# Optimization experiments

Measured on AMD Instinct MI355X. Metric: run time of the kernel, lower is better.

Reference implementation:

```python
import jax, jax.numpy as jnp
import numpy as np

B, N, F, C, HD = 16, 2048, 1024, 256, 64  # batch, points, feat_dims, channels, head dim
EPS_BN = 1e-5

def conv1d(w, x, b=None):
    # 1x1 Conv1d: w [O,C], x [B,C,N] -> [B,O,N]
    y = jnp.einsum('oc,bcn->bon', w, x)
    return y if b is None else y + b[None, :, None]

def batchnorm(x, g, b):
    # training-mode BN over (batch, length) per channel, biased variance
    m = x.mean(axis=(0, 2), keepdims=True)
    v = x.var(axis=(0, 2), keepdims=True)
    return g[None, :, None] * (x - m) * jax.lax.rsqrt(v + EPS_BN) + b[None, :, None]

def leaky(x):
    return jnp.where(x > 0, x, 0.2 * x)

def oa_layer(x, qk_w, qk_b, v_w, v_b, t_w, t_b, bn_g, bn_b):
    # x: [B,256,N]; q and k share weights (q_conv.weight = k_conv.weight)
    q = conv1d(qk_w, x, qk_b).transpose(0, 2, 1)      # [B,N,64]
    k = conv1d(qk_w, x, qk_b)                         # [B,64,N]
    v = conv1d(v_w, x, v_b)                           # [B,256,N]
    energy = jnp.einsum('bnc,bcm->bnm', q, k)         # [B,N,N]
    att = jax.nn.softmax(energy, axis=-1)
    att = att / (1e-9 + att.sum(axis=1, keepdims=True))  # L1 renorm over columns
    x_r = jnp.einsum('bcn,bnm->bcm', v, att)          # [B,256,N]
    x_r = leaky(batchnorm(conv1d(t_w, x - x_r, t_b), bn_g, bn_b))
    return x + x_r

def setup_inputs() -> dict:
    key = jax.random.key(0)
    ks = jax.random.split(key, 20)
    s = lambda fan: 1.0 / np.sqrt(fan)
    inp = {
        'feature': jax.random.normal(ks[0], (B, 1, F), jnp.float32),
        'prior': jax.random.normal(ks[1], (B, 3, N), jnp.float32),
        'mlp_w': jax.random.normal(ks[2], (C, F + 3), jnp.float32) * s(F + 3),
        'mlp_b': jax.random.normal(ks[3], (C,), jnp.float32) * 0.01,
        'qk_w': jax.random.normal(ks[4], (4, HD, C), jnp.float32) * s(C),
        'qk_b': jax.random.normal(ks[5], (4, HD), jnp.float32) * 0.01,
        'v_w': jax.random.normal(ks[6], (4, C, C), jnp.float32) * s(C),
        'v_b': jax.random.normal(ks[7], (4, C), jnp.float32) * 0.01,
        't_w': jax.random.normal(ks[8], (4, C, C), jnp.float32) * s(C),
        't_b': jax.random.normal(ks[9], (4, C), jnp.float32) * 0.01,
        'bn_g': jnp.ones((4, C), jnp.float32),
        'bn_b': jnp.zeros((4, C), jnp.float32),
        'dc1_w': jax.random.normal(ks[10], (C, 4 * C), jnp.float32) * s(4 * C),
        'dc1_bn_g': jnp.ones((C,), jnp.float32),
        'dc1_bn_b': jnp.zeros((C,), jnp.float32),
        'dc2_w': jax.random.normal(ks[11], (3, C), jnp.float32) * s(C),
        'dc2_b': jax.random.normal(ks[12], (3,), jnp.float32) * 0.01,
        'dc2_bn_g': jnp.ones((3,), jnp.float32),
        'dc2_bn_b': jnp.zeros((3,), jnp.float32),
    }
    return inp

def reference(feature, prior, mlp_w, mlp_b, qk_w, qk_b, v_w, v_b, t_w, t_b,
              bn_g, bn_b, dc1_w, dc1_bn_g, dc1_bn_b, dc2_w, dc2_b,
              dc2_bn_g, dc2_bn_b):
    n = prior.shape[2]
    feat = jnp.broadcast_to(feature.transpose(0, 2, 1), (feature.shape[0], feature.shape[2], n))
    p = conv1d(mlp_w, jnp.concatenate([feat, prior], axis=1), mlp_b)  # [B,256,N]
    outs = []
    for i in range(4):
        p = oa_layer(p, qk_w[i], qk_b[i], v_w[i], v_b[i], t_w[i], t_b[i], bn_g[i], bn_b[i])
        outs.append(p)
    pc = jnp.concatenate(outs, axis=1)                                # [B,1024,N]
    h = leaky(batchnorm(conv1d(dc1_w, pc), dc1_bn_g, dc1_bn_b))
    points = jnp.tanh(batchnorm(conv1d(dc2_w, h, dc2_b), dc2_bn_g, dc2_bn_b))
    return points.transpose(0, 2, 1)                                  # [B,N,3]
```

## Files before the change

### kernel.cpp

```cpp
#include <hip/hip_runtime.h>
#include <hip/hip_bf16.h>

typedef __hip_bfloat16 bf16;
typedef unsigned short ushort_t;

constexpr int kB = 16;
constexpr int kN = 2048;
constexpr int kF = 1024;
constexpr int kC = 256;
constexpr int kH = 64;

using f32x4 = __attribute__((ext_vector_type(4))) float;
using bf16x8 = __attribute__((ext_vector_type(8))) short;

__device__ __forceinline__ float us2f(unsigned short u) {
  union { unsigned int i; float f; } w;
  w.i = ((unsigned int)u) << 16;
  return w.f;
}
__device__ __forceinline__ unsigned short f2bu(float f) {
  union { bf16 h; unsigned short s; } u;
  u.h = __float2bfloat16(f);
  return u.s;
}

__global__ __launch_bounds__(256) void k_fb(const float* __restrict__ feat,
                                            const float* __restrict__ mlp_w,
                                            const float* __restrict__ mlp_b,
                                            float* __restrict__ fb) {
  const int b = blockIdx.x >> 8;
  const int c = blockIdx.x & 255;
  const int t = threadIdx.x;
  const float* wr = mlp_w + (size_t)c * (kF + 3);
  const float* fr = feat + (size_t)b * kF;
  float s = 0.f;
  for (int f = t; f < kF; f += 256) s += wr[f] * fr[f];
  __shared__ float red[256];
  red[t] = s;
  __syncthreads();
  for (int k = 128; k > 0; k >>= 1) {
    if (t < k) red[t] += red[t + k];
    __syncthreads();
  }
  if (t == 0) fb[blockIdx.x] = red[0] + mlp_b[c];
}

__global__ __launch_bounds__(256) void k_p0(const float* __restrict__ prior,
                                            const float* __restrict__ mlp_w,
                                            const float* __restrict__ fb,
                                            ushort_t* __restrict__ psh,
                                            ushort_t* __restrict__ psl) {
  const size_t i = (size_t)blockIdx.x * 256 + threadIdx.x;
  const int c = (int)(i & 255);
  const int n = (int)((i >> 8) & 2047);
  const int b = (int)(i >> 19);
  const float* wr = mlp_w + (size_t)c * (kF + 3) + kF;
  const float* pr = prior + (size_t)b * 3 * kN + n;
  const float v = fb[b * kC + c] + wr[0] * pr[0] + wr[1] * pr[kN] + wr[2] * pr[2 * kN];
  const ushort_t h = f2bu(v);
  psh[i] = h;
  psl[i] = f2bu(v - us2f(h));
}

__global__ __launch_bounds__(256) void k_wsplit(const float* __restrict__ qk_w,
                                                const float* __restrict__ v_w,
                                                const float* __restrict__ t_w,
                                                const float* __restrict__ dc1_w,
                                                ushort_t* __restrict__ wfh,
                                                ushort_t* __restrict__ wfl) {
  const int idx = blockIdx.x * 256 + threadIdx.x;
  const float* src;
  int stride, OS_;
  size_t dstoff;
  int g;
  if (idx < 8192) {
    const int l = idx >> 11; g = idx & 2047;
    src = qk_w + (size_t)l * 64 * 256; stride = 256; OS_ = 4;
    dstoff = (size_t)l * 16384;
  } else if (idx < 40960) {
    const int i2 = idx - 8192; const int l = i2 >> 13; g = i2 & 8191;
    src = v_w + (size_t)l * 256 * 256; stride = 256; OS_ = 16;
    dstoff = 65536 + (size_t)l * 65536;
  } else if (idx < 73728) {
    const int i2 = idx - 40960; const int l = i2 >> 13; g = i2 & 8191;
    src = t_w + (size_t)l * 256 * 256; stride = 256; OS_ = 16;
    dstoff = 327680 + (size_t)l * 65536;
  } else {
    const int i2 = idx - 73728; const int l = i2 >> 13; g = i2 & 8191;
    src = dc1_w + (size_t)l * 256; stride = 1024; OS_ = 16;
    dstoff = 589824 + (size_t)l * 65536;
  }
  const int kk = g / (OS_ * 64);
  const int rem = g % (OS_ * 64);
  const int osub = rem >> 6;
  const int lane = rem & 63;
  const int o = osub * 16 + (lane & 15);
  const int c = kk * 32 + (lane >> 4) * 8;
  const float* sp = src + (size_t)o * stride + c;
  ushort_t h[8], l8[8];
#pragma unroll
  for (int j = 0; j < 8; ++j) {
    const float v = sp[j];
    h[j] = f2bu(v);
    l8[j] = f2bu(v - us2f(h[j]));
  }
  *(uint4*)(wfh + dstoff + (size_t)g * 8) = *(const uint4*)h;
  *(uint4*)(wfl + dstoff + (size_t)g * 8) = *(const uint4*)l8;
}

__global__ __launch_bounds__(256) void k_qv(
    const ushort_t* __restrict__ xh, const ushort_t* __restrict__ xl,
    const ushort_t* __restrict__ wqh, const ushort_t* __restrict__ wql,
    const ushort_t* __restrict__ wvh, const ushort_t* __restrict__ wvl,
    const float* __restrict__ qbias, const float* __restrict__ vbias,
    ushort_t* __restrict__ Qh, ushort_t* __restrict__ Ql,
    bf16* __restrict__ Vo) {
  const int t = threadIdx.x;
  const int b = blockIdx.y;
  const int n0 = blockIdx.x * 64;
  const int lane = t & 63, wv = t >> 6;
  const int fr = lane & 15, fq = lane >> 4;
  const ushort_t* xbh = xh + ((size_t)b * kN + n0) * kC;
  const ushort_t* xbl = xl + ((size_t)b * kN + n0) * kC;
  f32x4 accq[4];
  f32x4 accv[4][4];
#pragma unroll
  for (int ns = 0; ns < 4; ++ns) {
    accq[ns] = (f32x4){0.f, 0.f, 0.f, 0.f};
#pragma unroll
    for (int s = 0; s < 4; ++s) accv[s][ns] = (f32x4){0.f, 0.f, 0.f, 0.f};
  }
  for (int kk = 0; kk < 8; ++kk) {
    bf16x8 bh[4], bl[4];
#pragma unroll
    for (int ns = 0; ns < 4; ++ns) {
      const size_t xi = (size_t)(ns * 16 + fr) * kC + kk * 32 + fq * 8;
      bh[ns] = *(const bf16x8*)(xbh + xi);
      bl[ns] = *(const bf16x8*)(xbl + xi);
    }
    {
      const size_t wi = (((size_t)kk * 4 + wv) * 64 + lane) * 8;
      const bf16x8 ah = *(const bf16x8*)(wqh + wi);
      const bf16x8 al = *(const bf16x8*)(wql + wi);
#pragma unroll
      for (int ns = 0; ns < 4; ++ns) {
        accq[ns] = __builtin_amdgcn_mfma_f32_16x16x32_bf16(ah, bh[ns], accq[ns], 0, 0, 0);
        accq[ns] = __builtin_amdgcn_mfma_f32_16x16x32_bf16(ah, bl[ns], accq[ns], 0, 0, 0);
        accq[ns] = __builtin_amdgcn_mfma_f32_16x16x32_bf16(al, bh[ns], accq[ns], 0, 0, 0);
      }
    }
#pragma unroll
    for (int s = 0; s < 4; ++s) {
      const size_t wi = (((size_t)kk * 16 + wv * 4 + s) * 64 + lane) * 8;
      const bf16x8 ah = *(const bf16x8*)(wvh + wi);
      const bf16x8 al = *(const bf16x8*)(wvl + wi);
#pragma unroll
      for (int ns = 0; ns < 4; ++ns) {
        accv[s][ns] = __builtin_amdgcn_mfma_f32_16x16x32_bf16(ah, bh[ns], accv[s][ns], 0, 0, 0);
        accv[s][ns] = __builtin_amdgcn_mfma_f32_16x16x32_bf16(ah, bl[ns], accv[s][ns], 0, 0, 0);
        accv[s][ns] = __builtin_amdgcn_mfma_f32_16x16x32_bf16(al, bh[ns], accv[s][ns], 0, 0, 0);
      }
    }
  }
  {
    const int o0 = wv * 16 + fq * 4;
#pragma unroll
    for (int ns = 0; ns < 4; ++ns) {
      const int n = n0 + ns * 16 + fr;
      ushort_t h4[4], l4[4];
#pragma unroll
      for (int r = 0; r < 4; ++r) {
        const float v = accq[ns][r] + qbias[o0 + r];
        h4[r] = f2bu(v);
        l4[r] = f2bu(v - us2f(h4[r]));
      }
      *(ushort4*)(Qh + ((size_t)b * kN + n) * kH + o0) = *(const ushort4*)h4;
      *(ushort4*)(Ql + ((size_t)b * kN + n) * kH + o0) = *(const ushort4*)l4;
    }
  }
#pragma unroll
  for (int s = 0; s < 4; ++s) {
    const int o0 = (wv * 4 + s) * 16 + fq * 4;
#pragma unroll
    for (int ns = 0; ns < 4; ++ns) {
      const int n = n0 + ns * 16 + fr;
#pragma unroll
      for (int r = 0; r < 4; ++r)
        Vo[((size_t)b * kC + o0 + r) * kN + n] = __float2bfloat16(accv[s][ns][r] + vbias[o0 + r]);
    }
  }
}

template <int O, int MODE>
__global__ __launch_bounds__(256) void k_conv(
    const ushort_t* __restrict__ xh, const ushort_t* __restrict__ xl,
    const ushort_t* __restrict__ wfh, const ushort_t* __restrict__ wfl,
    const float* __restrict__ bias,
    ushort_t* __restrict__ o1, ushort_t* __restrict__ o2,
    float* __restrict__ of) {
  constexpr int KK = 8;
  constexpr int OS = O / 16;
  constexpr int OSW = OS / 4;
  const int t = threadIdx.x;
  const int b = blockIdx.y;
  const int n0 = blockIdx.x * 64;
  const int lane = t & 63, wv = t >> 6;
  const int fr = lane & 15, fq = lane >> 4;
  const ushort_t* xbh = xh + ((size_t)b * kN + n0) * kC;
  const ushort_t* xbl = xl + ((size_t)b * kN + n0) * kC;
  f32x4 acc[OSW][4];
#pragma unroll
  for (int s = 0; s < OSW; ++s)
#pragma unroll
    for (int ns = 0; ns < 4; ++ns) acc[s][ns] = (f32x4){0.f, 0.f, 0.f, 0.f};
  for (int kk = 0; kk < KK; ++kk) {
    bf16x8 bh[4], bl[4];
#pragma unroll
    for (int ns = 0; ns < 4; ++ns) {
      const size_t xi = (size_t)(ns * 16 + fr) * kC + kk * 32 + fq * 8;
      bh[ns] = *(const bf16x8*)(xbh + xi);
      bl[ns] = *(const bf16x8*)(xbl + xi);
    }
#pragma unroll
    for (int s = 0; s < OSW; ++s) {
      const size_t wi = (((size_t)kk * OS + wv * OSW + s) * 64 + lane) * 8;
      const bf16x8 ah = *(const bf16x8*)(wfh + wi);
      const bf16x8 al = *(const bf16x8*)(wfl + wi);
#pragma unroll
      for (int ns = 0; ns < 4; ++ns) {
        acc[s][ns] = __builtin_amdgcn_mfma_f32_16x16x32_bf16(ah, bh[ns], acc[s][ns], 0, 0, 0);
        acc[s][ns] = __builtin_amdgcn_mfma_f32_16x16x32_bf16(ah, bl[ns], acc[s][ns], 0, 0, 0);
        acc[s][ns] = __builtin_amdgcn_mfma_f32_16x16x32_bf16(al, bh[ns], acc[s][ns], 0, 0, 0);
      }
    }
  }
  if (MODE == 2) {
    const int blk = blockIdx.y * gridDim.x + blockIdx.x;
#pragma unroll
    for (int s = 0; s < OSW; ++s) {
      const int o0 = (wv * OSW + s) * 16 + fq * 4;
      float yv[4][4];
#pragma unroll
      for (int ns = 0; ns < 4; ++ns) {
        const int n = n0 + ns * 16 + fr;
        const size_t idx = ((size_t)b * kN + n) * kC + o0;
        ushort_t h4[4], l4[4];
#pragma unroll
        for (int r = 0; r < 4; ++r) {
          const float y = acc[s][ns][r] + bias[o0 + r];
          yv[ns][r] = y;
          h4[r] = f2bu(y);
          l4[r] = f2bu(y - us2f(h4[r]));
        }
        *(ushort4*)(o1 + idx) = *(const ushort4*)h4;
        *(ushort4*)(o2 + idx) = *(const ushort4*)l4;
      }
#pragma unroll
      for (int r = 0; r < 4; ++r) {
        float s1 = yv[0][r] + yv[1][r] + yv[2][r] + yv[3][r];
        float s2 = yv[0][r] * yv[0][r] + yv[1][r] * yv[1][r] +
                   yv[2][r] * yv[2][r] + yv[3][r] * yv[3][r];
#pragma unroll
        for (int mask = 1; mask < 16; mask <<= 1) {
          s1 += __shfl_xor(s1, mask);
          s2 += __shfl_xor(s2, mask);
        }
        if (fr == 0) {
          of[(size_t)(o0 + r) * 512 + blk] = s1;
          of[131072 + (size_t)(o0 + r) * 512 + blk] = s2;
        }
      }
    }
  } else {
#pragma unroll
    for (int s = 0; s < OSW; ++s) {
      const int o0 = (wv * OSW + s) * 16 + fq * 4;
#pragma unroll
      for (int ns = 0; ns < 4; ++ns) {
        const int n = n0 + ns * 16 + fr;
#pragma unroll
        for (int r = 0; r < 4; ++r) {
          float* pp = of + ((size_t)b * kC + o0 + r) * kN + n;
          *pp = *pp + acc[s][ns][r];
        }
      }
    }
  }
}

__global__ __launch_bounds__(128) void k_bnred(const float* __restrict__ part,
                                               const float* __restrict__ g,
                                               const float* __restrict__ bb,
                                               float* __restrict__ af,
                                               float* __restrict__ cf) {
  const int c = blockIdx.x, t = threadIdx.x;
  const float4 v1 = *(const float4*)&part[(size_t)c * 512 + t * 4];
  const float4 v2 = *(const float4*)&part[131072 + (size_t)c * 512 + t * 4];
  float s1 = v1.x + v1.y + v1.z + v1.w;
  float s2 = v2.x + v2.y + v2.z + v2.w;
  __shared__ float r1[128], r2[128];
  r1[t] = s1;
  r2[t] = s2;
  __syncthreads();
  for (int k = 64; k > 0; k >>= 1) {
    if (t < k) {
      r1[t] += r1[t + k];
      r2[t] += r2[t + k];
    }
    __syncthreads();
  }
  if (t == 0) {
    const float im = 1.f / (float)(kB * kN);
    const float m = r1[0] * im;
    const float var = r2[0] * im - m * m;
    const float a = g[c] * rsqrtf(var + 1e-5f);
    af[c] = a;
    cf[c] = bb[c] - a * m;
  }
}

__global__ __launch_bounds__(256) void k_bnapply2(const ushort_t* __restrict__ yh,
                                                  const ushort_t* __restrict__ yl,
                                                  ushort_t* __restrict__ ph,
                                                  ushort_t* __restrict__ pl,
                                                  const float* __restrict__ af,
                                                  const float* __restrict__ cf) {
  const size_t i = ((size_t)blockIdx.x * 256 + threadIdx.x) * 4;
  const int c0 = (int)(i & 255);
  const ushort4 yh4 = *(const ushort4*)(yh + i);
  const ushort4 yl4 = *(const ushort4*)(yl + i);
  const ushort4 ph4 = *(const ushort4*)(ph + i);
  const ushort4 pl4 = *(const ushort4*)(pl + i);
  const float4 a4 = *(const float4*)(af + c0);
  const float4 c4 = *(const float4*)(cf + c0);
  const float y0 = us2f(yh4.x) + us2f(yl4.x);
  const float y1 = us2f(yh4.y) + us2f(yl4.y);
  const float y2 = us2f(yh4.z) + us2f(yl4.z);
  const float y3 = us2f(yh4.w) + us2f(yl4.w);
  float z0 = a4.x * y0 + c4.x; z0 = z0 > 0.f ? z0 : 0.2f * z0;
  float z1 = a4.y * y1 + c4.y; z1 = z1 > 0.f ? z1 : 0.2f * z1;
  float z2 = a4.z * y2 + c4.z; z2 = z2 > 0.f ? z2 : 0.2f * z2;
  float z3 = a4.w * y3 + c4.w; z3 = z3 > 0.f ? z3 : 0.2f * z3;
  const float p0 = us2f(ph4.x) + us2f(pl4.x) + z0;
  const float p1 = us2f(ph4.y) + us2f(pl4.y) + z1;
  const float p2 = us2f(ph4.z) + us2f(pl4.z) + z2;
  const float p3 = us2f(ph4.w) + us2f(pl4.w) + z3;
  ushort4 nh, nl;
  nh.x = f2bu(p0); nl.x = f2bu(p0 - us2f(nh.x));
  nh.y = f2bu(p1); nl.y = f2bu(p1 - us2f(nh.y));
  nh.z = f2bu(p2); nl.z = f2bu(p2 - us2f(nh.z));
  nh.w = f2bu(p3); nl.w = f2bu(p3 - us2f(nh.w));
  *(ushort4*)(ph + i) = nh;
  *(ushort4*)(pl + i) = nl;
}

__global__ __launch_bounds__(256) void k_rowstats(const ushort_t* __restrict__ Qhi,
                                                  const ushort_t* __restrict__ Qlo,
                                                  float* __restrict__ rmx,
                                                  float* __restrict__ rsn) {
  __shared__ __align__(16) ushort_t Bh[2][64][72];
  __shared__ __align__(16) ushort_t Bl[2][64][72];
  const int b = blockIdx.y, t = threadIdx.x;
  const int r0 = blockIdx.x * 64;
  const int lane = t & 63, w = t >> 6;
  const int fr = lane & 15, fq = lane >> 4;
  const size_t qbase = (size_t)b * kN * kH;
  bf16x8 ah0, ah1, al0, al1;
  {
    const ushort_t* qh = Qhi + qbase + (size_t)(r0 + w * 16 + fr) * kH;
    const ushort_t* ql = Qlo + qbase + (size_t)(r0 + w * 16 + fr) * kH;
    ah0 = *(const bf16x8*)(qh + fq * 8);
    ah1 = *(const bf16x8*)(qh + 32 + fq * 8);
    al0 = *(const bf16x8*)(ql + fq * 8);
    al1 = *(const bf16x8*)(ql + 32 + fq * 8);
  }
  float mx[4] = {-3.0e38f, -3.0e38f, -3.0e38f, -3.0e38f};
  float sm[4] = {0.f, 0.f, 0.f, 0.f};
  const int srow = t >> 2, scol = (t & 3) * 16;
  {
    const ushort_t* qh = Qhi + qbase + (size_t)srow * kH + scol;
    const ushort_t* ql = Qlo + qbase + (size_t)srow * kH + scol;
    *(uint4*)&Bh[0][srow][scol] = *(const uint4*)qh;
    *(uint4*)&Bh[0][srow][scol + 8] = *(const uint4*)(qh + 8);
    *(uint4*)&Bl[0][srow][scol] = *(const uint4*)ql;
    *(uint4*)&Bl[0][srow][scol + 8] = *(const uint4*)(ql + 8);
  }
  __syncthreads();
  int cur = 0;
  for (int m0 = 0; m0 < kN; m0 += 64) {
    uint4 rh0, rh1, rl0, rl1;
    const bool pf = (m0 + 64 < kN);
    if (pf) {
      const ushort_t* qh = Qhi + qbase + (size_t)(m0 + 64 + srow) * kH + scol;
      const ushort_t* ql = Qlo + qbase + (size_t)(m0 + 64 + srow) * kH + scol;
      rh0 = *(const uint4*)qh;
      rh1 = *(const uint4*)(qh + 8);
      rl0 = *(const uint4*)ql;
      rl1 = *(const uint4*)(ql + 8);
    }
    float ev[4][4];
#pragma unroll
    for (int cs = 0; cs < 4; ++cs) {
      const bf16x8 bh0 = *(const bf16x8*)&Bh[cur][cs * 16 + fr][fq * 8];
      const bf16x8 bh1 = *(const bf16x8*)&Bh[cur][cs * 16 + fr][32 + fq * 8];
      const bf16x8 bl0 = *(const bf16x8*)&Bl[cur][cs * 16 + fr][fq * 8];
      const bf16x8 bl1 = *(const bf16x8*)&Bl[cur][cs * 16 + fr][32 + fq * 8];
      f32x4 e = {0.f, 0.f, 0.f, 0.f};
      e = __builtin_amdgcn_mfma_f32_16x16x32_bf16(ah0, bh0, e, 0, 0, 0);
      e = __builtin_amdgcn_mfma_f32_16x16x32_bf16(ah1, bh1, e, 0, 0, 0);
      e = __builtin_amdgcn_mfma_f32_16x16x32_bf16(ah0, bl0, e, 0, 0, 0);
      e = __builtin_amdgcn_mfma_f32_16x16x32_bf16(ah1, bl1, e, 0, 0, 0);
      e = __builtin_amdgcn_mfma_f32_16x16x32_bf16(al0, bh0, e, 0, 0, 0);
      e = __builtin_amdgcn_mfma_f32_16x16x32_bf16(al1, bh1, e, 0, 0, 0);
      ev[cs][0] = e[0]; ev[cs][1] = e[1]; ev[cs][2] = e[2]; ev[cs][3] = e[3];
    }
#pragma unroll
    for (int r = 0; r < 4; ++r) {
      const float tmax = fmaxf(fmaxf(ev[0][r], ev[1][r]), fmaxf(ev[2][r], ev[3][r]));
      const float nm = fmaxf(mx[r], tmax);
      sm[r] = sm[r] * __expf(mx[r] - nm) + __expf(ev[0][r] - nm) + __expf(ev[1][r] - nm) +
              __expf(ev[2][r] - nm) + __expf(ev[3][r] - nm);
      mx[r] = nm;
    }
    if (pf) {
      *(uint4*)&Bh[cur ^ 1][srow][scol] = rh0;
      *(uint4*)&Bh[cur ^ 1][srow][scol + 8] = rh1;
      *(uint4*)&Bl[cur ^ 1][srow][scol] = rl0;
      *(uint4*)&Bl[cur ^ 1][srow][scol + 8] = rl1;
    }
    __syncthreads();
    cur ^= 1;
  }
#pragma unroll
  for (int mask = 1; mask < 16; mask <<= 1) {
#pragma unroll
    for (int r = 0; r < 4; ++r) {
      const float om = __shfl_xor(mx[r], mask);
      const float os = __shfl_xor(sm[r], mask);
      const float nm = fmaxf(mx[r], om);
      sm[r] = sm[r] * __expf(mx[r] - nm) + os * __expf(om - nm);
      mx[r] = nm;
    }
  }
  if (fr == 0) {
#pragma unroll
    for (int r = 0; r < 4; ++r) {
      const int row = r0 + w * 16 + fq * 4 + r;
      rmx[(size_t)b * kN + row] = mx[r];
      rsn[(size_t)b * kN + row] = 1.f / sm[r];
    }
  }
}

__global__ __launch_bounds__(256) void k_colpass(const ushort_t* __restrict__ Qhi,
                                                 const ushort_t* __restrict__ Qlo,
                                                 const bf16* __restrict__ V,
                                                 const float* __restrict__ rmx,
                                                 const float* __restrict__ rsn,
                                                 const ushort_t* __restrict__ psh,
                                                 const ushort_t* __restrict__ psl,
                                                 ushort_t* __restrict__ ush,
                                                 ushort_t* __restrict__ usl) {
  constexpr int MT = 64, NT = 32;
  __shared__ __align__(16) ushort_t Anh[2][NT][72];
  __shared__ __align__(16) ushort_t Anl[2][NT][72];
  __shared__ __align__(16) ushort_t Vs[2][kC][40];
  __shared__ __align__(16) ushort_t Pl[MT][40];
  __shared__ float CsI[MT];
  const int t = threadIdx.x;
  const int b = blockIdx.y;
  const int mBase = blockIdx.x * MT;
  const size_t qbase = (size_t)b * kN * kH;
  const ushort_t* Vb_ = (const ushort_t*)V + (size_t)b * kC * kN;
  const int lane = t & 63, wv = t >> 6;
  const int fr = lane & 15, fq = lane >> 4;
  bf16x8 bmh0, bmh1, bml0, bml1;
  {
    const ushort_t* qh = Qhi + qbase + (size_t)(mBase + wv * 16 + fr) * kH;
    const ushort_t* ql = Qlo + qbase + (size_t)(mBase + wv * 16 + fr) * kH;
    bmh0 = *(const bf16x8*)(qh + fq * 8);
    bmh1 = *(const bf16x8*)(qh + 32 + fq * 8);
    bml0 = *(const bf16x8*)(ql + fq * 8);
    bml1 = *(const bf16x8*)(ql + 32 + fq * 8);
  }
  f32x4 acc[4][4];
#pragma unroll
  for (int i = 0; i < 4; ++i)
#pragma unroll
    for (int j = 0; j < 4; ++j) acc[i][j] = (f32x4){0.f, 0.f, 0.f, 0.f};
  float csloc = 0.f;
  const int arow = t >> 3, acol = (t & 7) * 8;
  const int vc = t >> 2, vq = t & 3;
  {
    *(uint4*)&Anh[0][arow][acol] = *(const uint4*)(Qhi + qbase + (size_t)arow * kH + acol);
    *(uint4*)&Anl[0][arow][acol] = *(const uint4*)(Qlo + qbase + (size_t)arow * kH + acol);
#pragma unroll
    for (int it = 0; it < 4; ++it) {
      const int c = it * 64 + vc;
      *(uint4*)&Vs[0][c][vq * 8] = *(const uint4*)(Vb_ + (size_t)c * kN + vq * 8);
    }
  }
  __syncthreads();
  int cur = 0;
  for (int n0 = 0; n0 < kN; n0 += NT) {
    uint4 rAh, rAl, rV0, rV1, rV2, rV3;
    const bool pf = (n0 + NT < kN);
    if (pf) {
      const int nn = n0 + NT;
      rAh = *(const uint4*)(Qhi + qbase + (size_t)(nn + arow) * kH + acol);
      rAl = *(const uint4*)(Qlo + qbase + (size_t)(nn + arow) * kH + acol);
      rV0 = *(const uint4*)(Vb_ + (size_t)(0 * 64 + vc) * kN + nn + vq * 8);
      rV1 = *(const uint4*)(Vb_ + (size_t)(1 * 64 + vc) * kN + nn + vq * 8);
      rV2 = *(const uint4*)(Vb_ + (size_t)(2 * 64 + vc) * kN + nn + vq * 8);
      rV3 = *(const uint4*)(Vb_ + (size_t)(3 * 64 + vc) * kN + nn + vq * 8);
    }
    const float4 rm0 = *(const float4*)&rmx[(size_t)b * kN + n0 + fq * 4];
    const float4 rm1 = *(const float4*)&rmx[(size_t)b * kN + n0 + 16 + fq * 4];
    const float4 rs0 = *(const float4*)&rsn[(size_t)b * kN + n0 + fq * 4];
    const float4 rs1 = *(const float4*)&rsn[(size_t)b * kN + n0 + 16 + fq * 4];
#pragma unroll
    for (int ns = 0; ns < 2; ++ns) {
      const bf16x8 ah0 = *(const bf16x8*)&Anh[cur][ns * 16 + fr][fq * 8];
      const bf16x8 ah1 = *(const bf16x8*)&Anh[cur][ns * 16 + fr][32 + fq * 8];
      const bf16x8 al0 = *(const bf16x8*)&Anl[cur][ns * 16 + fr][fq * 8];
      const bf16x8 al1 = *(const bf16x8*)&Anl[cur][ns * 16 + fr][32 + fq * 8];
      f32x4 e = {0.f, 0.f, 0.f, 0.f};
      e = __builtin_amdgcn_mfma_f32_16x16x32_bf16(ah0, bmh0, e, 0, 0, 0);
      e = __builtin_amdgcn_mfma_f32_16x16x32_bf16(ah1, bmh1, e, 0, 0, 0);
      e = __builtin_amdgcn_mfma_f32_16x16x32_bf16(ah0, bml0, e, 0, 0, 0);
      e = __builtin_amdgcn_mfma_f32_16x16x32_bf16(ah1, bml1, e, 0, 0, 0);
      e = __builtin_amdgcn_mfma_f32_16x16x32_bf16(al0, bmh0, e, 0, 0, 0);
      e = __builtin_amdgcn_mfma_f32_16x16x32_bf16(al1, bmh1, e, 0, 0, 0);
      const float4 rm = ns ? rm1 : rm0;
      const float4 rs = ns ? rs1 : rs0;
      ushort_t p4[4];
      {
        const float p0 = __expf(e[0] - rm.x) * rs.x;
        const float p1 = __expf(e[1] - rm.y) * rs.y;
        const float p2 = __expf(e[2] - rm.z) * rs.z;
        const float p3 = __expf(e[3] - rm.w) * rs.w;
        p4[0] = f2bu(p0); p4[1] = f2bu(p1); p4[2] = f2bu(p2); p4[3] = f2bu(p3);
        csloc += p0 + p1 + p2 + p3;
      }
      *(ushort4*)&Pl[wv * 16 + fr][ns * 16 + fq * 4] = *(const ushort4*)p4;
    }
    __syncthreads();
    bf16x8 am[4], bv[4];
#pragma unroll
    for (int ms = 0; ms < 4; ++ms)
      am[ms] = *(const bf16x8*)&Pl[ms * 16 + fr][fq * 8];
#pragma unroll
    for (int cs = 0; cs < 4; ++cs)
      bv[cs] = *(const bf16x8*)&Vs[cur][wv * 64 + cs * 16 + fr][fq * 8];
#pragma unroll
    for (int ms = 0; ms < 4; ++ms)
#pragma unroll
      for (int cs = 0; cs < 4; ++cs)
        acc[ms][cs] = __builtin_amdgcn_mfma_f32_16x16x32_bf16(am[ms], bv[cs], acc[ms][cs], 0, 0, 0);
    if (pf) {
      *(uint4*)&Anh[cur ^ 1][arow][acol] = rAh;
      *(uint4*)&Anl[cur ^ 1][arow][acol] = rAl;
      *(uint4*)&Vs[cur ^ 1][0 * 64 + vc][vq * 8] = rV0;
      *(uint4*)&Vs[cur ^ 1][1 * 64 + vc][vq * 8] = rV1;
      *(uint4*)&Vs[cur ^ 1][2 * 64 + vc][vq * 8] = rV2;
      *(uint4*)&Vs[cur ^ 1][3 * 64 + vc][vq * 8] = rV3;
    }
    __syncthreads();
    cur ^= 1;
  }
  csloc += __shfl_xor(csloc, 16);
  csloc += __shfl_xor(csloc, 32);
  if (fq == 0) CsI[wv * 16 + fr] = 1.f / (1e-9f + csloc);
  __syncthreads();
#pragma unroll
  for (int ms = 0; ms < 4; ++ms) {
#pragma unroll
    for (int r = 0; r < 4; ++r) {
      const int ml = ms * 16 + fq * 4 + r;
      const float inv = CsI[ml];
      const size_t row = ((size_t)b * kN + mBase + ml) * kC;
#pragma unroll
      for (int cs = 0; cs < 4; ++cs) {
        const int c = wv * 64 + cs * 16 + fr;
        const float xv = us2f(psh[row + c]) + us2f(psl[row + c]);
        const float u = xv - acc[ms][cs][r] * inv;
        const ushort_t h = f2bu(u);
        ush[row + c] = h;
        usl[row + c] = f2bu(u - us2f(h));
      }
    }
  }
}

__global__ __launch_bounds__(256) void k_bnstats(const float* __restrict__ y, int nch,
                                                 float* __restrict__ mean,
                                                 float* __restrict__ rsig) {
  const int c = blockIdx.x, t = threadIdx.x;
  float s = 0.f, s2 = 0.f;
  for (int b = 0; b < kB; ++b) {
    const float* p = y + ((size_t)b * nch + c) * kN;
    for (int n = t; n < kN; n += 256) {
      const float v = p[n];
      s += v;
      s2 += v * v;
    }
  }
  __shared__ float r1[256], r2[256];
  r1[t] = s;
  r2[t] = s2;
  __syncthreads();
  for (int k = 128; k > 0; k >>= 1) {
    if (t < k) {
      r1[t] += r1[t + k];
      r2[t] += r2[t + k];
    }
    __syncthreads();
  }
  if (t == 0) {
    const float im = 1.f / (float)(kB * kN);
    const float m = r1[0] * im;
    const float var = r2[0] * im - m * m;
    mean[c] = m;
    rsig[c] = rsqrtf(var + 1e-5f);
  }
}

__global__ __launch_bounds__(256) void k_dc2(const float* __restrict__ h,
                                             const float* __restrict__ mean,
                                             const float* __restrict__ rsig,
                                             const float* __restrict__ g,
                                             const float* __restrict__ bb,
                                             const float* __restrict__ w,
                                             const float* __restrict__ d2b,
                                             float* __restrict__ tpre) {
  __shared__ float wS[3][kC];
  __shared__ float aS[kC], cS[kC];
  const int t = threadIdx.x, b = blockIdx.y;
  const int n = blockIdx.x * 256 + t;
  {
    const float a = g[t] * rsig[t];
    aS[t] = a;
    cS[t] = bb[t] - a * mean[t];
    wS[0][t] = w[t];
    wS[1][t] = w[kC + t];
    wS[2][t] = w[2 * kC + t];
  }
  __syncthreads();
  float a0 = d2b[0], a1 = d2b[1], a2 = d2b[2];
  const float* hb = h + (size_t)b * kC * kN + n;
  for (int c = 0; c < kC; ++c) {
    float z = hb[(size_t)c * kN] * aS[c] + cS[c];
    z = z > 0.f ? z : 0.2f * z;
    a0 += wS[0][c] * z;
    a1 += wS[1][c] * z;
    a2 += wS[2][c] * z;
  }
  tpre[((size_t)b * 3 + 0) * kN + n] = a0;
  tpre[((size_t)b * 3 + 1) * kN + n] = a1;
  tpre[((size_t)b * 3 + 2) * kN + n] = a2;
}

__global__ __launch_bounds__(256) void k_final(const float* __restrict__ tpre,
                                               const float* __restrict__ mean,
                                               const float* __restrict__ rsig,
                                               const float* __restrict__ g,
                                               const float* __restrict__ bb,
                                               float* __restrict__ out) {
  const int i = blockIdx.x * 256 + threadIdx.x;
  const int n = i & (kN - 1), b = i >> 11;
#pragma unroll
  for (int j = 0; j < 3; ++j) {
    const float v = tpre[((size_t)b * 3 + j) * kN + n];
    const float z = g[j] * (v - mean[j]) * rsig[j] + bb[j];
    out[(size_t)i * 3 + j] = tanhf(z);
  }
}

extern "C" void kernel_launch(void* const* d_in, const int* in_sizes, int n_in,
                              void* d_out, int out_size, void* d_ws, size_t ws_size,
                              hipStream_t stream) {
  const float* feature  = (const float*)d_in[0];
  const float* prior    = (const float*)d_in[1];
  const float* mlp_w    = (const float*)d_in[2];
  const float* mlp_b    = (const float*)d_in[3];
  const float* qk_w     = (const float*)d_in[4];
  const float* qk_b     = (const float*)d_in[5];
  const float* v_w      = (const float*)d_in[6];
  const float* v_b      = (const float*)d_in[7];
  const float* t_w      = (const float*)d_in[8];
  const float* t_b      = (const float*)d_in[9];
  const float* bn_g     = (const float*)d_in[10];
  const float* bn_b     = (const float*)d_in[11];
  const float* dc1_w    = (const float*)d_in[12];
  const float* dc1_bn_g = (const float*)d_in[13];
  const float* dc1_bn_b = (const float*)d_in[14];
  const float* dc2_w    = (const float*)d_in[15];
  const float* dc2_b    = (const float*)d_in[16];
  const float* dc2_bn_g = (const float*)d_in[17];
  const float* dc2_bn_b = (const float*)d_in[18];
  float* out = (float*)d_out;

  char* base = (char*)d_ws;
  size_t off = 0;
  auto carve = [&](size_t bytes) {
    char* p = base + off;
    off += (bytes + 255) & ~(size_t)255;
    return p;
  };
  const size_t ne = (size_t)kB * kN * kC;
  ushort_t* psh  = (ushort_t*)carve(ne * 2);
  ushort_t* psl  = (ushort_t*)carve(ne * 2);
  ushort_t* ush  = (ushort_t*)carve(ne * 2);
  ushort_t* usl  = (ushort_t*)carve(ne * 2);
  float*    hacc = (float*)carve(ne * 4);
  ushort_t* Qhi  = (ushort_t*)carve((size_t)kB * kN * kH * 2);
  ushort_t* Qlo  = (ushort_t*)carve((size_t)kB * kN * kH * 2);
  bf16*     Vb   = (bf16*)carve(ne * 2);
  ushort_t* wfh  = (ushort_t*)carve((size_t)851968 * 2);
  ushort_t* wfl  = (ushort_t*)carve((size_t)851968 * 2);
  float*    part = (float*)carve((size_t)2 * 131072 * 4);
  float*    rmx  = (float*)carve((size_t)kB * kN * 4);
  float*    rsn  = (float*)carve((size_t)kB * kN * 4);
  float*    fb   = (float*)carve((size_t)kB * kC * 4);
  float*    bnm  = (float*)carve(kC * 4);
  float*    bnr  = (float*)carve(kC * 4);
  float*    tpre = (float*)carve((size_t)kB * 3 * kN * 4);

  hipMemsetAsync(hacc, 0, ne * 4, stream);
  k_wsplit<<<416, 256, 0, stream>>>(qk_w, v_w, t_w, dc1_w, wfh, wfl);
  k_fb<<<kB * kC, 256, 0, stream>>>(feature, mlp_w, mlp_b, fb);
  k_p0<<<(int)(ne / 256), 256, 0, stream>>>(prior, mlp_w, fb, psh, psl);

  const dim3 gC(kN / 64, kB);
  for (int l = 0; l < 4; ++l) {
    const size_t qk_off  = (size_t)l * 16384;
    const size_t v_off   = 65536 + (size_t)l * 65536;
    const size_t t_off   = 327680 + (size_t)l * 65536;
    const size_t dc1_off = 589824 + (size_t)l * 65536;
    k_qv<<<gC, 256, 0, stream>>>(psh, psl, wfh + qk_off, wfl + qk_off,
                                 wfh + v_off, wfl + v_off,
                                 qk_b + l * kH, v_b + l * kC, Qhi, Qlo, Vb);
    k_rowstats<<<gC, 256, 0, stream>>>(Qhi, Qlo, rmx, rsn);
    k_colpass<<<gC, 256, 0, stream>>>(Qhi, Qlo, Vb, rmx, rsn, psh, psl, ush, usl);
    k_conv<256, 2><<<gC, 256, 0, stream>>>(ush, usl, wfh + t_off, wfl + t_off,
                                           t_b + l * kC, ush, usl, part);
    k_bnred<<<kC, 128, 0, stream>>>(part, bn_g + l * kC, bn_b + l * kC, bnm, bnr);
    k_bnapply2<<<(int)(ne / 4 / 256), 256, 0, stream>>>(ush, usl, psh, psl, bnm, bnr);
    k_conv<256, 4><<<gC, 256, 0, stream>>>(psh, psl, wfh + dc1_off, wfl + dc1_off,
                                           nullptr, nullptr, nullptr, hacc);
  }

  k_bnstats<<<kC, 256, 0, stream>>>(hacc, kC, bnm, bnr);
  k_dc2<<<dim3(kN / 256, kB), 256, 0, stream>>>(hacc, bnm, bnr, dc1_bn_g, dc1_bn_b,
                                                dc2_w, dc2_b, tpre);
  k_bnstats<<<3, 256, 0, stream>>>(tpre, 3, bnm, bnr);
  k_final<<<(kB * kN) / 256, 256, 0, stream>>>(tpre, bnm, bnr, dc2_bn_g, dc2_bn_b, out);
}
```

Before: 1.234 ms.

## Fuse BN-apply residual, dc1 conv, and next-layer QV projection into one kernel

Replaces the separate BN-apply, dc1 conv and next-layer Q/V projection kernels with one fused kernel. Each block computes the updated residual in registers, feeds it straight into the MFMA GEMMs for dc1 and for the next layer's Q/V, and has one wave write the updated p back. This removes a full read/write pass over the activations and two launches per layer. In exchange the fused kernel holds many accumulators (Q, V and dc1), so register pressure rises and occupancy may drop.

```diff
diff --git a/kernel.cpp b/kernel.cpp
--- a/kernel.cpp
+++ b/kernel.cpp
@@ -191,16 +191,158 @@
   }
 }
 
-template <int O, int MODE>
-__global__ __launch_bounds__(256) void k_conv(
+template <int HASQV>
+__global__ __launch_bounds__(256, 2) void k_fuse(
+    const ushort_t* __restrict__ yh, const ushort_t* __restrict__ yl,
+    ushort_t* __restrict__ ph, ushort_t* __restrict__ pl,
+    const float* __restrict__ af, const float* __restrict__ cf,
+    const ushort_t* __restrict__ wqh, const ushort_t* __restrict__ wql,
+    const ushort_t* __restrict__ wvh, const ushort_t* __restrict__ wvl,
+    const ushort_t* __restrict__ wdh, const ushort_t* __restrict__ wdl,
+    const float* __restrict__ qbias, const float* __restrict__ vbias,
+    ushort_t* __restrict__ Qh, ushort_t* __restrict__ Ql,
+    bf16* __restrict__ Vo, float* __restrict__ hacc) {
+  const int t = threadIdx.x;
+  const int b = blockIdx.y;
+  const int n0 = blockIdx.x * 64;
+  const int lane = t & 63, wv = t >> 6;
+  const int fr = lane & 15, fq = lane >> 4;
+  const size_t rowbase = ((size_t)b * kN + n0) * kC;
+  f32x4 accq[4];
+  f32x4 accv[4][4];
+  f32x4 accd[4][4];
+#pragma unroll
+  for (int ns = 0; ns < 4; ++ns) {
+    accq[ns] = (f32x4){0.f, 0.f, 0.f, 0.f};
+#pragma unroll
+    for (int s = 0; s < 4; ++s) {
+      accv[s][ns] = (f32x4){0.f, 0.f, 0.f, 0.f};
+      accd[s][ns] = (f32x4){0.f, 0.f, 0.f, 0.f};
+    }
+  }
+  for (int kk = 0; kk < 8; ++kk) {
+    const int cbase = kk * 32 + fq * 8;
+    const float4 a4a = *(const float4*)(af + cbase);
+    const float4 a4b = *(const float4*)(af + cbase + 4);
+    const float4 c4a = *(const float4*)(cf + cbase);
+    const float4 c4b = *(const float4*)(cf + cbase + 4);
+    const float av[8] = {a4a.x, a4a.y, a4a.z, a4a.w, a4b.x, a4b.y, a4b.z, a4b.w};
+    const float cv[8] = {c4a.x, c4a.y, c4a.z, c4a.w, c4b.x, c4b.y, c4b.z, c4b.w};
+    bf16x8 bh[4], bl[4];
+#pragma unroll
+    for (int ns = 0; ns < 4; ++ns) {
+      const size_t idx = rowbase + (size_t)(ns * 16 + fr) * kC + cbase;
+      ushort_t yh8[8], yl8[8], p8h[8], p8l[8], nh8[8], nl8[8];
+      *(uint4*)yh8 = *(const uint4*)(yh + idx);
+      *(uint4*)yl8 = *(const uint4*)(yl + idx);
+      *(uint4*)p8h = *(const uint4*)(ph + idx);
+      *(uint4*)p8l = *(const uint4*)(pl + idx);
+#pragma unroll
+      for (int j = 0; j < 8; ++j) {
+        const float yv = us2f(yh8[j]) + us2f(yl8[j]);
+        float z = av[j] * yv + cv[j];
+        z = z > 0.f ? z : 0.2f * z;
+        const float pv = us2f(p8h[j]) + us2f(p8l[j]) + z;
+        nh8[j] = f2bu(pv);
+        nl8[j] = f2bu(pv - us2f(nh8[j]));
+      }
+      bh[ns] = *(const bf16x8*)nh8;
+      bl[ns] = *(const bf16x8*)nl8;
+    }
+    __syncthreads();
+    if (wv == 0) {
+#pragma unroll
+      for (int ns = 0; ns < 4; ++ns) {
+        const size_t idx = rowbase + (size_t)(ns * 16 + fr) * kC + cbase;
+        *(uint4*)(ph + idx) = *(const uint4*)&bh[ns];
+        *(uint4*)(pl + idx) = *(const uint4*)&bl[ns];
+      }
+    }
+    if (HASQV) {
+      const size_t wi = (((size_t)kk * 4 + wv) * 64 + lane) * 8;
+      const bf16x8 ah = *(const bf16x8*)(wqh + wi);
+      const bf16x8 al = *(const bf16x8*)(wql + wi);
+#pragma unroll
+      for (int ns = 0; ns < 4; ++ns) {
+        accq[ns] = __builtin_amdgcn_mfma_f32_16x16x32_bf16(ah, bh[ns], accq[ns], 0, 0, 0);
+        accq[ns] = __builtin_amdgcn_mfma_f32_16x16x32_bf16(ah, bl[ns], accq[ns], 0, 0, 0);
+        accq[ns] = __builtin_amdgcn_mfma_f32_16x16x32_bf16(al, bh[ns], accq[ns], 0, 0, 0);
+      }
+#pragma unroll
+      for (int s = 0; s < 4; ++s) {
+        const size_t wi2 = (((size_t)kk * 16 + wv * 4 + s) * 64 + lane) * 8;
+        const bf16x8 vh = *(const bf16x8*)(wvh + wi2);
+        const bf16x8 vl = *(const bf16x8*)(wvl + wi2);
+#pragma unroll
+        for (int ns = 0; ns < 4; ++ns) {
+          accv[s][ns] = __builtin_amdgcn_mfma_f32_16x16x32_bf16(vh, bh[ns], accv[s][ns], 0, 0, 0);
+          accv[s][ns] = __builtin_amdgcn_mfma_f32_16x16x32_bf16(vh, bl[ns], accv[s][ns], 0, 0, 0);
+          accv[s][ns] = __builtin_amdgcn_mfma_f32_16x16x32_bf16(vl, bh[ns], accv[s][ns], 0, 0, 0);
+        }
+      }
+    }
+#pragma unroll
+    for (int s = 0; s < 4; ++s) {
+      const size_t wi3 = (((size_t)kk * 16 + wv * 4 + s) * 64 + lane) * 8;
+      const bf16x8 dh = *(const bf16x8*)(wdh + wi3);
+      const bf16x8 dl = *(const bf16x8*)(wdl + wi3);
+#pragma unroll
+      for (int ns = 0; ns < 4; ++ns) {
+        accd[s][ns] = __builtin_amdgcn_mfma_f32_16x16x32_bf16(dh, bh[ns], accd[s][ns], 0, 0, 0);
+        accd[s][ns] = __builtin_amdgcn_mfma_f32_16x16x32_bf16(dh, bl[ns], accd[s][ns], 0, 0, 0);
+        accd[s][ns] = __builtin_amdgcn_mfma_f32_16x16x32_bf16(dl, bh[ns], accd[s][ns], 0, 0, 0);
+      }
+    }
+  }
+  if (HASQV) {
+    const int o0 = wv * 16 + fq * 4;
+#pragma unroll
+    for (int ns = 0; ns < 4; ++ns) {
+      const int n = n0 + ns * 16 + fr;
+      ushort_t h4[4], l4[4];
+#pragma unroll
+      for (int r = 0; r < 4; ++r) {
+        const float v = accq[ns][r] + qbias[o0 + r];
+        h4[r] = f2bu(v);
+        l4[r] = f2bu(v - us2f(h4[r]));
+      }
+      *(ushort4*)(Qh + ((size_t)b * kN + n) * kH + o0) = *(const ushort4*)h4;
+      *(ushort4*)(Ql + ((size_t)b * kN + n) * kH + o0) = *(const ushort4*)l4;
+    }
+#pragma unroll
+    for (int s = 0; s < 4; ++s) {
+      const int oV = (wv * 4 + s) * 16 + fq * 4;
+#pragma unroll
+      for (int ns = 0; ns < 4; ++ns) {
+        const int n = n0 + ns * 16 + fr;
+#pragma unroll
+        for (int r = 0; r < 4; ++r)
+          Vo[((size_t)b * kC + oV + r) * kN + n] =
+              __float2bfloat16(accv[s][ns][r] + vbias[oV + r]);
+      }
+    }
+  }
+#pragma unroll
+  for (int s = 0; s < 4; ++s) {
+    const int oD = (wv * 4 + s) * 16 + fq * 4;
+#pragma unroll
+    for (int ns = 0; ns < 4; ++ns) {
+      const int n = n0 + ns * 16 + fr;
+#pragma unroll
+      for (int r = 0; r < 4; ++r) {
+        float* pp = hacc + ((size_t)b * kC + oD + r) * kN + n;
+        *pp = *pp + accd[s][ns][r];
+      }
+    }
+  }
+}
+
+__global__ __launch_bounds__(256) void k_tconv(
     const ushort_t* __restrict__ xh, const ushort_t* __restrict__ xl,
     const ushort_t* __restrict__ wfh, const ushort_t* __restrict__ wfl,
     const float* __restrict__ bias,
     ushort_t* __restrict__ o1, ushort_t* __restrict__ o2,
     float* __restrict__ of) {
-  constexpr int KK = 8;
-  constexpr int OS = O / 16;
-  constexpr int OSW = OS / 4;
   const int t = threadIdx.x;
   const int b = blockIdx.y;
   const int n0 = blockIdx.x * 64;
@@ -208,12 +350,12 @@
   const int fr = lane & 15, fq = lane >> 4;
   const ushort_t* xbh = xh + ((size_t)b * kN + n0) * kC;
   const ushort_t* xbl = xl + ((size_t)b * kN + n0) * kC;
-  f32x4 acc[OSW][4];
-#pragma unroll
-  for (int s = 0; s < OSW; ++s)
+  f32x4 acc[4][4];
+#pragma unroll
+  for (int s = 0; s < 4; ++s)
 #pragma unroll
     for (int ns = 0; ns < 4; ++ns) acc[s][ns] = (f32x4){0.f, 0.f, 0.f, 0.f};
-  for (int kk = 0; kk < KK; ++kk) {
+  for (int kk = 0; kk < 8; ++kk) {
     bf16x8 bh[4], bl[4];
 #pragma unroll
     for (int ns = 0; ns < 4; ++ns) {
@@ -222,8 +364,8 @@
       bl[ns] = *(const bf16x8*)(xbl + xi);
     }
 #pragma unroll
-    for (int s = 0; s < OSW; ++s) {
-      const size_t wi = (((size_t)kk * OS + wv * OSW + s) * 64 + lane) * 8;
+    for (int s = 0; s < 4; ++s) {
+      const size_t wi = (((size_t)kk * 16 + wv * 4 + s) * 64 + lane) * 8;
       const bf16x8 ah = *(const bf16x8*)(wfh + wi);
       const bf16x8 al = *(const bf16x8*)(wfl + wi);
 #pragma unroll
@@ -234,55 +376,40 @@
       }
     }
   }
-  if (MODE == 2) {
-    const int blk = blockIdx.y * gridDim.x + blockIdx.x;
-#pragma unroll
-    for (int s = 0; s < OSW; ++s) {
-      const int o0 = (wv * OSW + s) * 16 + fq * 4;
-      float yv[4][4];
-#pragma unroll
-      for (int ns = 0; ns < 4; ++ns) {
-        const int n = n0 + ns * 16 + fr;
-        const size_t idx = ((size_t)b * kN + n) * kC + o0;
-        ushort_t h4[4], l4[4];
-#pragma unroll
-        for (int r = 0; r < 4; ++r) {
-          const float y = acc[s][ns][r] + bias[o0 + r];
-          yv[ns][r] = y;
-          h4[r] = f2bu(y);
-          l4[r] = f2bu(y - us2f(h4[r]));
-        }
-        *(ushort4*)(o1 + idx) = *(const ushort4*)h4;
-        *(ushort4*)(o2 + idx) = *(const ushort4*)l4;
-      }
+  __syncthreads();
+  const int blk = blockIdx.y * gridDim.x + blockIdx.x;
+#pragma unroll
+  for (int s = 0; s < 4; ++s) {
+    const int o0 = (wv * 4 + s) * 16 + fq * 4;
+    float yv[4][4];
+#pragma unroll
+    for (int ns = 0; ns < 4; ++ns) {
+      const int n = n0 + ns * 16 + fr;
+      const size_t idx = ((size_t)b * kN + n) * kC + o0;
+      ushort_t h4[4], l4[4];
 #pragma unroll
       for (int r = 0; r < 4; ++r) {
-        float s1 = yv[0][r] + yv[1][r] + yv[2][r] + yv[3][r];
-        float s2 = yv[0][r] * yv[0][r] + yv[1][r] * yv[1][r] +
-                   yv[2][r] * yv[2][r] + yv[3][r] * yv[3][r];
-#pragma unroll
-        for (int mask = 1; mask < 16; mask <<= 1) {
-          s1 += __shfl_xor(s1, mask);
-          s2 += __shfl_xor(s2, mask);
-        }
-        if (fr == 0) {
-          of[(size_t)(o0 + r) * 512 + blk] = s1;
-          of[131072 + (size_t)(o0 + r) * 512 + blk] = s2;
-        }
-      }
-    }
-  } else {
-#pragma unroll
-    for (int s = 0; s < OSW; ++s) {
-      const int o0 = (wv * OSW + s) * 16 + fq * 4;
-#pragma unroll
-      for (int ns = 0; ns < 4; ++ns) {
-        const int n = n0 + ns * 16 + fr;
-#pragma unroll
-        for (int r = 0; r < 4; ++r) {
-          float* pp = of + ((size_t)b * kC + o0 + r) * kN + n;
-          *pp = *pp + acc[s][ns][r];
-        }
+        const float y = acc[s][ns][r] + bias[o0 + r];
+        yv[ns][r] = y;
+        h4[r] = f2bu(y);
+        l4[r] = f2bu(y - us2f(h4[r]));
+      }
+      *(ushort4*)(o1 + idx) = *(const ushort4*)h4;
+      *(ushort4*)(o2 + idx) = *(const ushort4*)l4;
+    }
+#pragma unroll
+    for (int r = 0; r < 4; ++r) {
+      float s1 = yv[0][r] + yv[1][r] + yv[2][r] + yv[3][r];
+      float s2 = yv[0][r] * yv[0][r] + yv[1][r] * yv[1][r] +
+                 yv[2][r] * yv[2][r] + yv[3][r] * yv[3][r];
+#pragma unroll
+      for (int mask = 1; mask < 16; mask <<= 1) {
+        s1 += __shfl_xor(s1, mask);
+        s2 += __shfl_xor(s2, mask);
+      }
+      if (fr == 0) {
+        of[(size_t)(o0 + r) * 512 + blk] = s1;
+        of[131072 + (size_t)(o0 + r) * 512 + blk] = s2;
       }
     }
   }
@@ -317,41 +444,6 @@
     af[c] = a;
     cf[c] = bb[c] - a * m;
   }
-}
-
-__global__ __launch_bounds__(256) void k_bnapply2(const ushort_t* __restrict__ yh,
-                                                  const ushort_t* __restrict__ yl,
-                                                  ushort_t* __restrict__ ph,
-                                                  ushort_t* __restrict__ pl,
-                                                  const float* __restrict__ af,
-                                                  const float* __restrict__ cf) {
-  const size_t i = ((size_t)blockIdx.x * 256 + threadIdx.x) * 4;
-  const int c0 = (int)(i & 255);
-  const ushort4 yh4 = *(const ushort4*)(yh + i);
-  const ushort4 yl4 = *(const ushort4*)(yl + i);
-  const ushort4 ph4 = *(const ushort4*)(ph + i);
-  const ushort4 pl4 = *(const ushort4*)(pl + i);
-  const float4 a4 = *(const float4*)(af + c0);
-  const float4 c4 = *(const float4*)(cf + c0);
-  const float y0 = us2f(yh4.x) + us2f(yl4.x);
-  const float y1 = us2f(yh4.y) + us2f(yl4.y);
-  const float y2 = us2f(yh4.z) + us2f(yl4.z);
-  const float y3 = us2f(yh4.w) + us2f(yl4.w);
-  float z0 = a4.x * y0 + c4.x; z0 = z0 > 0.f ? z0 : 0.2f * z0;
-  float z1 = a4.y * y1 + c4.y; z1 = z1 > 0.f ? z1 : 0.2f * z1;
-  float z2 = a4.z * y2 + c4.z; z2 = z2 > 0.f ? z2 : 0.2f * z2;
-  float z3 = a4.w * y3 + c4.w; z3 = z3 > 0.f ? z3 : 0.2f * z3;
-  const float p0 = us2f(ph4.x) + us2f(pl4.x) + z0;
-  const float p1 = us2f(ph4.y) + us2f(pl4.y) + z1;
-  const float p2 = us2f(ph4.z) + us2f(pl4.z) + z2;
-  const float p3 = us2f(ph4.w) + us2f(pl4.w) + z3;
-  ushort4 nh, nl;
-  nh.x = f2bu(p0); nl.x = f2bu(p0 - us2f(nh.x));
-  nh.y = f2bu(p1); nl.y = f2bu(p1 - us2f(nh.y));
-  nh.z = f2bu(p2); nl.z = f2bu(p2 - us2f(nh.z));
-  nh.w = f2bu(p3); nl.w = f2bu(p3 - us2f(nh.w));
-  *(ushort4*)(ph + i) = nh;
-  *(ushort4*)(pl + i) = nl;
 }
 
 __global__ __launch_bounds__(256) void k_rowstats(const ushort_t* __restrict__ Qhi,
@@ -732,22 +824,32 @@
   k_p0<<<(int)(ne / 256), 256, 0, stream>>>(prior, mlp_w, fb, psh, psl);
 
   const dim3 gC(kN / 64, kB);
+  k_qv<<<gC, 256, 0, stream>>>(psh, psl, wfh, wfl, wfh + 65536, wfl + 65536,
+                               qk_b, v_b, Qhi, Qlo, Vb);
   for (int l = 0; l < 4; ++l) {
-    const size_t qk_off  = (size_t)l * 16384;
-    const size_t v_off   = 65536 + (size_t)l * 65536;
     const size_t t_off   = 327680 + (size_t)l * 65536;
     const size_t dc1_off = 589824 + (size_t)l * 65536;
-    k_qv<<<gC, 256, 0, stream>>>(psh, psl, wfh + qk_off, wfl + qk_off,
-                                 wfh + v_off, wfl + v_off,
-                                 qk_b + l * kH, v_b + l * kC, Qhi, Qlo, Vb);
     k_rowstats<<<gC, 256, 0, stream>>>(Qhi, Qlo, rmx, rsn);
     k_colpass<<<gC, 256, 0, stream>>>(Qhi, Qlo, Vb, rmx, rsn, psh, psl, ush, usl);
-    k_conv<256, 2><<<gC, 256, 0, stream>>>(ush, usl, wfh + t_off, wfl + t_off,
-                                           t_b + l * kC, ush, usl, part);
+    k_tconv<<<gC, 256, 0, stream>>>(ush, usl, wfh + t_off, wfl + t_off,
+                                    t_b + l * kC, ush, usl, part);
     k_bnred<<<kC, 128, 0, stream>>>(part, bn_g + l * kC, bn_b + l * kC, bnm, bnr);
-    k_bnapply2<<<(int)(ne / 4 / 256), 256, 0, stream>>>(ush, usl, psh, psl, bnm, bnr);
-    k_conv<256, 4><<<gC, 256, 0, stream>>>(psh, psl, wfh + dc1_off, wfl + dc1_off,
-                                           nullptr, nullptr, nullptr, hacc);
+    if (l < 3) {
+      const size_t qk_n = (size_t)(l + 1) * 16384;
+      const size_t v_n  = 65536 + (size_t)(l + 1) * 65536;
+      k_fuse<1><<<gC, 256, 0, stream>>>(ush, usl, psh, psl, bnm, bnr,
+                                        wfh + qk_n, wfl + qk_n,
+                                        wfh + v_n, wfl + v_n,
+                                        wfh + dc1_off, wfl + dc1_off,
+                                        qk_b + (l + 1) * kH, v_b + (l + 1) * kC,
+                                        Qhi, Qlo, Vb, hacc);
+    } else {
+      k_fuse<0><<<gC, 256, 0, stream>>>(ush, usl, psh, psl, bnm, bnr,
+                                        nullptr, nullptr, nullptr, nullptr,
+                                        wfh + dc1_off, wfl + dc1_off,
+                                        nullptr, nullptr,
+                                        nullptr, nullptr, nullptr, hacc);
+    }
   }
 
   k_bnstats<<<kC, 256, 0, stream>>>(hacc, kC, bnm, bnr);
```

New measurement: 1.183 ms. -4.1%, faster.
